# Performance work log

Measured on AMD Instinct MI355X. Metric: run time of the kernel, lower is better.

The kernel has to match this reference:

```python
import jax, jax.numpy as jnp
import numpy as np

N_NODES = 50000
N_EDGES = 800000
F_IN = 128
F_OUT = 128
EPS_STD = 1e-5  # PyG StdAggregation epsilon


def setup_inputs() -> dict:
    key = jax.random.key(0)
    ks = jax.random.split(key, 8)
    x = jax.random.normal(ks[0], (N_NODES, F_IN), dtype=jnp.float32)
    edge_index = jax.random.randint(ks[1], (2, N_EDGES), 0, N_NODES, dtype=jnp.int64)
    s = 0.02
    # pre_nn: Linear(2*F_IN -> F_IN)
    W_pre = jax.random.normal(ks[2], (2 * F_IN, F_IN), dtype=jnp.float32) * s
    b_pre = jnp.zeros((F_IN,), dtype=jnp.float32)
    # post_nn: Linear((1 + 4 aggregators * 1 scaler) * F_IN -> F_OUT)
    W_post = jax.random.normal(ks[3], (5 * F_IN, F_OUT), dtype=jnp.float32) * s
    b_post = jnp.zeros((F_OUT,), dtype=jnp.float32)
    # final lin: Linear(F_OUT -> F_OUT)
    W_lin = jax.random.normal(ks[4], (F_OUT, F_OUT), dtype=jnp.float32) * s
    b_lin = jnp.zeros((F_OUT,), dtype=jnp.float32)
    return {"x": x, "W_pre": W_pre, "b_pre": b_pre, "W_post": W_post,
            "b_post": b_post, "W_lin": W_lin, "b_lin": b_lin,
            "edge_index": edge_index}


def _pna_forward(x, W_pre, b_pre, W_post, b_post, W_lin, b_lin, edge_index):
    N = x.shape[0]
    src = edge_index[0]  # x_j (source / neighbor)
    dst = edge_index[1]  # x_i (target / aggregation index)

    # per-edge message: Linear(cat(x_i, x_j))  [E, F_IN]
    h = jnp.concatenate([x[dst], x[src]], axis=-1) @ W_pre + b_pre

    ones = jnp.ones((h.shape[0],), dtype=h.dtype)
    deg = jax.ops.segment_sum(ones, dst, num_segments=N)          # in-degree [N]
    deg_c = jnp.maximum(deg, 1.0)[:, None]

    s1 = jax.ops.segment_sum(h, dst, num_segments=N)
    s2 = jax.ops.segment_sum(h * h, dst, num_segments=N)
    mean = s1 / deg_c
    var = jax.nn.relu(s2 / deg_c - mean * mean)
    std = jnp.sqrt(var + EPS_STD)

    has_nb = (deg > 0)[:, None]
    mx = jax.ops.segment_max(h, dst, num_segments=N)
    mn = jax.ops.segment_min(h, dst, num_segments=N)
    mx = jnp.where(has_nb, mx, 0.0)
    mn = jnp.where(has_nb, mn, 0.0)

    # aggregators in declared order: mean, max, min, std -> [N, 4*F_IN]
    agg = jnp.concatenate([mean, mx, mn, std], axis=-1)

    # 'linear' degree scaler: deg / avg_deg
    avg_deg = jnp.mean(deg)
    agg = agg * (deg[:, None] / avg_deg)

    out = jnp.concatenate([x, agg], axis=-1) @ W_post + b_post
    out = out @ W_lin + b_lin
    return jax.nn.relu(out)


def reference(x, W_pre, b_pre, W_post, b_post, W_lin, b_lin, edge_index):
    return _pna_forward(x, W_pre, b_pre, W_post, b_post, W_lin, b_lin, edge_index)
```

## Files before the change

kernel.cpp:

```cpp
#include <hip/hip_runtime.h>
#include <hip/hip_bf16.h>
#include <math.h>


typedef _Float16 f16;
typedef _Float16 f16x8 __attribute__((ext_vector_type(8)));
typedef _Float16 f16x2 __attribute__((ext_vector_type(2)));
typedef float    f32x4 __attribute__((ext_vector_type(4)));

__device__ __forceinline__ unsigned packh2(float a, float b) {
  union { unsigned u; f16x2 h; } x; x.h = (f16x2){(f16)a, (f16)b}; return x.u;
}
__device__ __forceinline__ float2 unpackh2(unsigned v) {
  union { unsigned u; f16x2 h; } x; x.u = v;
  return make_float2((float)x.h.x, (float)x.h.y);
}

template<int KTOT, int KO1, bool HASB, bool RELU, bool OUTF16>
__global__ __launch_bounds__(256) void gemm_reg_k(
    const f16* __restrict__ A1, const f16* __restrict__ A2,
    const f16* __restrict__ Wt, const float* __restrict__ bias,
    float* __restrict__ outF, f16* __restrict__ outH, int M, int ldOut)
{
  const int tid = threadIdx.x;
  const int l   = tid & 63;
  const int w   = tid >> 6;
  const int wr  = (w >> 1) * 32;
  const int wc  = (w & 1) * 64;
  const int li  = l & 15, kg = l >> 4;
  const int rowBase = blockIdx.x * 64;
  const int colBase = blockIdx.y * 128;
  constexpr int ld2 = (KTOT > KO1) ? (KTOT - KO1) : 1;

  int aOff[2], a2Off[2], bOff[4];
#pragma unroll
  for (int r = 0; r < 2; ++r) {
    int gr = rowBase + wr + r * 16 + li; if (gr > M - 1) gr = M - 1;
    aOff[r] = gr * KO1; a2Off[r] = gr * ld2;
  }
#pragma unroll
  for (int c = 0; c < 4; ++c) bOff[c] = (colBase + wc + c * 16 + li) * KTOT;

  f32x4 acc[2][4];
#pragma unroll
  for (int r = 0; r < 2; ++r)
#pragma unroll
    for (int c = 0; c < 4; ++c) acc[r][c] = (f32x4){0.f, 0.f, 0.f, 0.f};

  f16x8 aA[2], bA[4], aB[2], bB[4];
  auto lf = [&](int k0, f16x8 a[2], f16x8 b[4]) {
    int k = k0 + kg * 8;
    if (KO1 == KTOT || k0 < KO1) {
#pragma unroll
      for (int r = 0; r < 2; ++r) a[r] = *reinterpret_cast<const f16x8*>(A1 + aOff[r] + k);
    } else {
#pragma unroll
      for (int r = 0; r < 2; ++r) a[r] = *reinterpret_cast<const f16x8*>(A2 + a2Off[r] + (k - KO1));
    }
#pragma unroll
    for (int c = 0; c < 4; ++c) b[c] = *reinterpret_cast<const f16x8*>(Wt + bOff[c] + k);
  };

  lf(0, aA, bA);
  for (int k0 = 0; k0 < KTOT; k0 += 64) {
    lf(k0 + 32, aB, bB);
#pragma unroll
    for (int r = 0; r < 2; ++r)
#pragma unroll
      for (int c = 0; c < 4; ++c)
        acc[r][c] = __builtin_amdgcn_mfma_f32_16x16x32_f16(aA[r], bA[c], acc[r][c], 0, 0, 0);
    if (k0 + 64 < KTOT) lf(k0 + 64, aA, bA);
#pragma unroll
    for (int r = 0; r < 2; ++r)
#pragma unroll
      for (int c = 0; c < 4; ++c)
        acc[r][c] = __builtin_amdgcn_mfma_f32_16x16x32_f16(aB[r], bB[c], acc[r][c], 0, 0, 0);
  }

  float bv[4];
#pragma unroll
  for (int c = 0; c < 4; ++c) {
    int col = colBase + wc + c * 16 + li;
    bv[c] = (HASB && col < 128) ? bias[col] : 0.f;
  }

  if constexpr (OUTF16) {
    __shared__ __align__(16) f16 Ls[64][136];
#pragma unroll
    for (int c = 0; c < 4; ++c) {
      int col = wc + c * 16 + li;
#pragma unroll
      for (int r = 0; r < 2; ++r)
#pragma unroll
        for (int j = 0; j < 4; ++j) {
          float v = acc[r][c][j] + bv[c];
          if (RELU) v = fmaxf(v, 0.f);
          Ls[wr + r * 16 + kg * 4 + j][col] = (f16)v;
        }
    }
    __syncthreads();
#pragma unroll
    for (int i = 0; i < 4; ++i) {
      int s = tid + 256 * i;
      int rr = s >> 4, cc = (s & 15) * 8;
      int gr = rowBase + rr;
      if (gr < M)
        *reinterpret_cast<float4*>(&outH[(size_t)gr * ldOut + colBase + cc]) =
            *reinterpret_cast<const float4*>(&Ls[rr][cc]);
    }
  } else {
    __shared__ __align__(16) float Lf[64][132];
#pragma unroll
    for (int c = 0; c < 4; ++c) {
      int col = wc + c * 16 + li;
#pragma unroll
      for (int r = 0; r < 2; ++r)
#pragma unroll
        for (int j = 0; j < 4; ++j) {
          float v = acc[r][c][j] + bv[c];
          if (RELU) v = fmaxf(v, 0.f);
          Lf[wr + r * 16 + kg * 4 + j][col] = v;
        }
    }
    __syncthreads();
#pragma unroll
    for (int i = 0; i < 8; ++i) {
      int s = tid + 256 * i;
      int rr = s >> 5, cc = (s & 31) * 4;
      int gr = rowBase + rr;
      if (gr < M)
        *reinterpret_cast<float4*>(&outF[(size_t)gr * ldOut + colBase + cc]) =
            *reinterpret_cast<const float4*>(&Lf[rr][cc]);
    }
  }
}

__global__ void cvt_x_k(const float* __restrict__ x, f16* __restrict__ xf, int n) {
  int i = (blockIdx.x * 256 + threadIdx.x) * 4;
  if (i < n) {
    float4 v = *reinterpret_cast<const float4*>(&x[i]);
    xf[i] = (f16)v.x; xf[i + 1] = (f16)v.y; xf[i + 2] = (f16)v.z; xf[i + 3] = (f16)v.w;
  }
}

__global__ void prep_wpre_k(const float* __restrict__ W, f16* __restrict__ Wt) {
  int e = blockIdx.x * 256 + threadIdx.x;
  if (e < 256 * 128) {
    int n = e >> 7, k = e & 127;
    float v = (n < 128) ? W[(size_t)k * 128 + n] : W[(size_t)(128 + k) * 128 + (n - 128)];
    Wt[e] = (f16)v;
  }
}

__global__ void transp_w_k(const float* __restrict__ W, f16* __restrict__ Wt, int K) {
  int e = blockIdx.x * 256 + threadIdx.x;
  if (e < 128 * K) {
    int nn = e / K, kk = e - nn * K;
    Wt[e] = (f16)W[(size_t)kk * 128 + nn];
  }
}

__global__ void zero_k(int* __restrict__ p, int n) {
  int i = blockIdx.x * 256 + threadIdx.x;
  if (i < n) p[i] = 0;
}

__global__ void count_k(const int* __restrict__ ei, int* __restrict__ deg, int E) {
  int e = blockIdx.x * 256 + threadIdx.x;
  if (e < E) atomicAdd(&deg[ei[E + e]], 1);
}

__device__ __forceinline__ int blockExclScan(int v, int* wtot) {
  int lane = threadIdx.x & 63, wid = threadIdx.x >> 6;
  int x = v;
#pragma unroll
  for (int d = 1; d < 64; d <<= 1) {
    int y = __shfl_up(x, d);
    if (lane >= d) x += y;
  }
  if (lane == 63) wtot[wid] = x;
  __syncthreads();
  if (threadIdx.x == 0) {
    int s = 0;
#pragma unroll
    for (int k = 0; k < 4; ++k) { int t = wtot[k]; wtot[k] = s; s += t; }
  }
  __syncthreads();
  return wtot[wid] + x - v;
}

__global__ __launch_bounds__(256) void scan1_k(const int* __restrict__ deg,
                                               int* __restrict__ offs,
                                               int* __restrict__ partials, int n) {
  __shared__ int wtot[4];
  int i = blockIdx.x * 256 + threadIdx.x;
  int v = (i < n) ? deg[i] : 0;
  int e = blockExclScan(v, wtot);
  if (i < n) offs[i] = e;
  if (threadIdx.x == 255) partials[blockIdx.x] = e + v;
}

__global__ __launch_bounds__(256) void scan2_k(int* __restrict__ partials, int nb) {
  __shared__ int wtot[4];
  int v = (threadIdx.x < nb) ? partials[threadIdx.x] : 0;
  int e = blockExclScan(v, wtot);
  if (threadIdx.x < nb) partials[threadIdx.x] = e;
}

__global__ void scan3_k(const int* __restrict__ partials, int* __restrict__ offs,
                        int* __restrict__ cur, int n, int E) {
  int i = blockIdx.x * 256 + threadIdx.x;
  if (i < n) {
    int v = offs[i] + partials[i >> 8];
    offs[i] = v; cur[i] = v;
  }
  if (i == 0) offs[n] = E;
}

__global__ void scatter_k(const int* __restrict__ ei, int* __restrict__ cursor,
                          int* __restrict__ ssrc, int E) {
  int e = blockIdx.x * 256 + threadIdx.x;
  if (e < E) {
    int d = ei[E + e];
    int pos = atomicAdd(&cursor[d], 1);
    ssrc[pos] = ei[e];
  }
}

__global__ __launch_bounds__(256) void agg_k(
    const f16* __restrict__ CP, const int* __restrict__ offs,
    const int* __restrict__ ssrc, f16* __restrict__ AGG, int N)
{
  int w = threadIdx.x >> 6;
  int t = threadIdx.x & 63;
  int i = blockIdx.x * 4 + w;
  if (i >= N) return;
  int start = offs[i], end = offs[i + 1];
  int deg = end - start;
  unsigned* AGGu = (unsigned*)AGG;
  size_t o = (size_t)i * 256 + t;
  if (deg == 0) {
    AGGu[o] = 0u; AGGu[o + 64] = 0u; AGGu[o + 128] = 0u; AGGu[o + 192] = 0u;
    return;
  }
  const unsigned* CPu = (const unsigned*)CP;
  float s0 = 0.f, s1 = 0.f, q0 = 0.f, q1 = 0.f;
  float mx0 = -INFINITY, mx1 = -INFINITY, mn0 = INFINITY, mn1 = INFINITY;
  for (int base = start; base < end; base += 64) {
    int cnt = min(end - base, 64);
    int myidx = (base + t < end) ? ssrc[base + t] : 0;
    for (int j = 0; j < cnt; ++j) {
      int src = __shfl(myidx, j);
      float2 v = unpackh2(CPu[(size_t)src * 128 + 64 + t]);
      s0 += v.x; s1 += v.y;
      q0 += v.x * v.x; q1 += v.y * v.y;
      mx0 = fmaxf(mx0, v.x); mx1 = fmaxf(mx1, v.y);
      mn0 = fminf(mn0, v.x); mn1 = fminf(mn1, v.y);
    }
  }
  float2 c = unpackh2(CPu[(size_t)i * 128 + t]);
  float degf = (float)deg;
  float inv = 1.f / degf;
  float m10 = s0 * inv, m11 = s1 * inv;
  float var0 = fmaxf(q0 * inv - m10 * m10, 0.f);
  float var1 = fmaxf(q1 * inv - m11 * m11, 0.f);
  float sd0 = sqrtf(var0 + 1e-5f), sd1 = sqrtf(var1 + 1e-5f);
  float sc = degf * (1.0f / 16.0f);
  AGGu[o]       = packh2((c.x + m10) * sc, (c.y + m11) * sc);
  AGGu[o + 64]  = packh2((c.x + mx0) * sc, (c.y + mx1) * sc);
  AGGu[o + 128] = packh2((c.x + mn0) * sc, (c.y + mn1) * sc);
  AGGu[o + 192] = packh2(sd0 * sc, sd1 * sc);
}

extern "C" void kernel_launch(void* const* d_in, const int* in_sizes, int n_in,
                              void* d_out, int out_size, void* d_ws, size_t ws_size,
                              hipStream_t stream) {
  const float* x      = (const float*)d_in[0];
  const float* W_pre  = (const float*)d_in[1];
  const float* b_pre  = (const float*)d_in[2];
  const float* W_post = (const float*)d_in[3];
  const float* b_post = (const float*)d_in[4];
  const float* W_lin  = (const float*)d_in[5];
  const float* b_lin  = (const float*)d_in[6];
  const int*   ei     = (const int*)d_in[7];

  const int N = in_sizes[0] / 128;
  const int E = in_sizes[7] / 2;

  char* ws = (char*)d_ws;
  size_t off = 0;
  auto alloc = [&](size_t bytes) -> void* {
    void* p = ws + off; off += (bytes + 255) & ~(size_t)255; return p;
  };
  f16*   xf     = (f16*)  alloc((size_t)N * 128 * 2);
  f16*   CP     = (f16*)  alloc((size_t)N * 256 * 2);
  f16*   AGG    = (f16*)  alloc((size_t)N * 512 * 2);
  f16*   T1     = (f16*)  alloc((size_t)N * 128 * 2);
  f16*   WtPre  = (f16*)  alloc(256 * 128 * 2);
  f16*   WtPost = (f16*)  alloc(128 * 640 * 2);
  f16*   WtLin  = (f16*)  alloc(128 * 128 * 2);
  int*   ssrc   = (int*)  alloc((size_t)E * 4);
  int*   deg    = (int*)  alloc((size_t)N * 4);
  int*   offs   = (int*)  alloc((size_t)(N + 1) * 4);
  int*   cur    = (int*)  alloc((size_t)N * 4);
  int*   parts  = (int*)  alloc(1024 * 4);

  const int gTile = (N + 63) / 64;
  const int gE    = (E + 255) / 256;
  const int gN    = (N + 255) / 256;

  cvt_x_k<<<(N * 128 / 4 + 255) / 256, 256, 0, stream>>>(x, xf, N * 128);
  prep_wpre_k<<<(256 * 128 + 255) / 256, 256, 0, stream>>>(W_pre, WtPre);
  transp_w_k<<<(128 * 640 + 255) / 256, 256, 0, stream>>>(W_post, WtPost, 640);
  transp_w_k<<<(128 * 128 + 255) / 256, 256, 0, stream>>>(W_lin,  WtLin,  128);

  zero_k<<<gN, 256, 0, stream>>>(deg, N);

  gemm_reg_k<128, 128, true, false, true><<<dim3(gTile, 2), 256, 0, stream>>>(
      xf, nullptr, WtPre, b_pre, nullptr, CP, N, 256);

  count_k<<<gE, 256, 0, stream>>>(ei, deg, E);
  scan1_k<<<gN, 256, 0, stream>>>(deg, offs, parts, N);
  scan2_k<<<1, 256, 0, stream>>>(parts, gN);
  scan3_k<<<gN, 256, 0, stream>>>(parts, offs, cur, N, E);
  scatter_k<<<gE, 256, 0, stream>>>(ei, cur, ssrc, E);

  agg_k<<<(N + 3) / 4, 256, 0, stream>>>(CP, offs, ssrc, AGG, N);

  gemm_reg_k<640, 128, true, false, true><<<dim3(gTile, 1), 256, 0, stream>>>(
      xf, AGG, WtPost, b_post, nullptr, T1, N, 128);
  gemm_reg_k<128, 128, true, true, false><<<dim3(gTile, 1), 256, 0, stream>>>(
      T1, nullptr, WtLin, b_lin, (float*)d_out, nullptr, N, 128);
}
```

Measured before the change: 348.0 us.

## Fold post and final linear weights into one GEMM; unroll aggregation gathers

```diff
diff --git a/kernel.cpp b/kernel.cpp
--- a/kernel.cpp
+++ b/kernel.cpp
@@ -152,11 +152,22 @@
   }
 }
 
-__global__ void transp_w_k(const float* __restrict__ W, f16* __restrict__ Wt, int K) {
+__global__ void fold_w_k(const float* __restrict__ Wpost, const float* __restrict__ bpost,
+                         const float* __restrict__ Wlin,  const float* __restrict__ blin,
+                         f16* __restrict__ WtComb, float* __restrict__ bcomb) {
   int e = blockIdx.x * 256 + threadIdx.x;
-  if (e < 128 * K) {
-    int nn = e / K, kk = e - nn * K;
-    Wt[e] = (f16)W[(size_t)kk * 128 + nn];
+  if (e < 640 * 128) {
+    int n = e / 640, k = e - n * 640;
+    float s = 0.f;
+#pragma unroll 4
+    for (int m = 0; m < 128; ++m) s += Wpost[(size_t)k * 128 + m] * Wlin[(size_t)m * 128 + n];
+    WtComb[(size_t)n * 640 + k] = (f16)s;
+  } else if (e < 640 * 128 + 128) {
+    int n = e - 640 * 128;
+    float s = blin[n];
+#pragma unroll 4
+    for (int m = 0; m < 128; ++m) s += bpost[m] * Wlin[(size_t)m * 128 + n];
+    bcomb[n] = s;
   }
 }
 
@@ -246,18 +257,37 @@
   const unsigned* CPu = (const unsigned*)CP;
   float s0 = 0.f, s1 = 0.f, q0 = 0.f, q1 = 0.f;
   float mx0 = -INFINITY, mx1 = -INFINITY, mn0 = INFINITY, mn1 = INFINITY;
+
+  auto accum = [&](unsigned u) {
+    float2 v = unpackh2(u);
+    s0 += v.x; s1 += v.y;
+    q0 = fmaf(v.x, v.x, q0); q1 = fmaf(v.y, v.y, q1);
+    mx0 = fmaxf(mx0, v.x); mx1 = fmaxf(mx1, v.y);
+    mn0 = fminf(mn0, v.x); mn1 = fminf(mn1, v.y);
+  };
+
   for (int base = start; base < end; base += 64) {
     int cnt = min(end - base, 64);
-    int myidx = (base + t < end) ? ssrc[base + t] : 0;
-    for (int j = 0; j < cnt; ++j) {
-      int src = __shfl(myidx, j);
-      float2 v = unpackh2(CPu[(size_t)src * 128 + 64 + t]);
-      s0 += v.x; s1 += v.y;
-      q0 += v.x * v.x; q1 += v.y * v.y;
-      mx0 = fmaxf(mx0, v.x); mx1 = fmaxf(mx1, v.y);
-      mn0 = fminf(mn0, v.x); mn1 = fminf(mn1, v.y);
-    }
-  }
+    int myoff = 0;
+    if (base + t < end) myoff = ssrc[base + t] * 128 + 64;
+    int j = 0;
+    for (; j + 4 <= cnt; j += 4) {
+      int o0 = __shfl(myoff, j);
+      int o1 = __shfl(myoff, j + 1);
+      int o2 = __shfl(myoff, j + 2);
+      int o3 = __shfl(myoff, j + 3);
+      unsigned u0 = CPu[o0 + t];
+      unsigned u1 = CPu[o1 + t];
+      unsigned u2 = CPu[o2 + t];
+      unsigned u3 = CPu[o3 + t];
+      accum(u0); accum(u1); accum(u2); accum(u3);
+    }
+    for (; j < cnt; ++j) {
+      int o0 = __shfl(myoff, j);
+      accum(CPu[o0 + t]);
+    }
+  }
+
   float2 c = unpackh2(CPu[(size_t)i * 128 + t]);
   float degf = (float)deg;
   float inv = 1.f / degf;
@@ -295,10 +325,9 @@
   f16*   xf     = (f16*)  alloc((size_t)N * 128 * 2);
   f16*   CP     = (f16*)  alloc((size_t)N * 256 * 2);
   f16*   AGG    = (f16*)  alloc((size_t)N * 512 * 2);
-  f16*   T1     = (f16*)  alloc((size_t)N * 128 * 2);
   f16*   WtPre  = (f16*)  alloc(256 * 128 * 2);
-  f16*   WtPost = (f16*)  alloc(128 * 640 * 2);
-  f16*   WtLin  = (f16*)  alloc(128 * 128 * 2);
+  f16*   WtComb = (f16*)  alloc(128 * 640 * 2);
+  float* bcomb  = (float*)alloc(128 * 4);
   int*   ssrc   = (int*)  alloc((size_t)E * 4);
   int*   deg    = (int*)  alloc((size_t)N * 4);
   int*   offs   = (int*)  alloc((size_t)(N + 1) * 4);
@@ -311,8 +340,7 @@
 
   cvt_x_k<<<(N * 128 / 4 + 255) / 256, 256, 0, stream>>>(x, xf, N * 128);
   prep_wpre_k<<<(256 * 128 + 255) / 256, 256, 0, stream>>>(W_pre, WtPre);
-  transp_w_k<<<(128 * 640 + 255) / 256, 256, 0, stream>>>(W_post, WtPost, 640);
-  transp_w_k<<<(128 * 128 + 255) / 256, 256, 0, stream>>>(W_lin,  WtLin,  128);
+  fold_w_k<<<(640 * 128 + 128 + 255) / 256, 256, 0, stream>>>(W_post, b_post, W_lin, b_lin, WtComb, bcomb);
 
   zero_k<<<gN, 256, 0, stream>>>(deg, N);
 
@@ -327,8 +355,6 @@
 
   agg_k<<<(N + 3) / 4, 256, 0, stream>>>(CP, offs, ssrc, AGG, N);
 
-  gemm_reg_k<640, 128, true, false, true><<<dim3(gTile, 1), 256, 0, stream>>>(
-      xf, AGG, WtPost, b_post, nullptr, T1, N, 128);
-  gemm_reg_k<128, 128, true, true, false><<<dim3(gTile, 1), 256, 0, stream>>>(
-      T1, nullptr, WtLin, b_lin, (float*)d_out, nullptr, N, 128);
-}
+  gemm_reg_k<640, 128, true, true, false><<<dim3(gTile, 1), 256, 0, stream>>>(
+      xf, AGG, WtComb, bcomb, (float*)d_out, nullptr, N, 128);
+}
```

Result: faster. 312.7 us (-10.1%).
